# Optimization experiments

Measured on AMD Instinct MI355X. Metric: run time of the kernel, lower is better.

## Reference

```python
import jax, jax.numpy as jnp
import numpy as np

B, H, N, F, P, NODE = 64, 168, 512, 8, 24, 0


def _lstm(x, k, rk, b, return_sequences):
    # x: (B, T, Fin); keras LSTM gate order i, f, g(c), o
    Bx = x.shape[0]
    U = rk.shape[0]
    h0 = jnp.zeros((Bx, U), x.dtype)

    def step(carry, xt):
        h, c = carry
        z = xt @ k + h @ rk + b
        i, f, g, o = jnp.split(z, 4, axis=-1)
        c = jax.nn.sigmoid(f) * c + jax.nn.sigmoid(i) * jnp.tanh(g)
        h = jax.nn.sigmoid(o) * jnp.tanh(c)
        return (h, c), h

    (_, _), hs = jax.lax.scan(step, (h0, h0), jnp.swapaxes(x, 0, 1))
    return jnp.swapaxes(hs, 0, 1) if return_sequences else hs[-1]


def _node_summaries(inputs):
    # inputs: (B, H, N, F). Per-(b,n) temporal stats over H of feature 0.
    x0 = inputs[..., 0]                      # (B, H, N)
    mean_full = x0.mean(axis=1)              # (B, N)
    mean_half = x0[:, H // 2:].mean(axis=1)
    std_full = x0.std(axis=1)                # population std (ddof=0), like tf
    std_half = x0[:, H // 2:].std(axis=1)
    c = x0 - mean_full[:, None, :]
    m2 = (c * c).mean(axis=1)
    m3 = (c ** 3).mean(axis=1)
    m4 = (c ** 4).mean(axis=1)
    skew = jnp.nan_to_num(m3 / m2 ** 1.5)    # scipy.stats.skew (biased)
    kurt = jnp.nan_to_num(m4 / (m2 * m2) - 3.0)  # scipy Fisher kurtosis
    t = jnp.arange(H, dtype=x0.dtype)
    tc = t - t.mean()
    slope = jnp.nan_to_num(jnp.einsum('h,bhn->bn', tc, x0) / (tc * tc).sum())
    return jnp.stack([mean_full, mean_half, std_full, std_half, skew, kurt, slope], axis=2)  # (B, N, 7)


def reference(inputs, adj, w_gcn1, b_gcn1, w_gcn2, b_gcn2, w_conv1, b_conv1,
              w_conv2, b_conv2, k_lstm1, rk_lstm1, b_lstm1, k_lstm2, rk_lstm2,
              b_lstm2, w_out, b_out):
    nf = _node_summaries(inputs)                                   # (B, N, 7)
    # GraphConv: relu(A @ X @ W + b)
    h = jax.nn.relu(jnp.einsum('nm,bmc->bnc', adj, nf @ w_gcn1) + b_gcn1)
    g = jax.nn.relu(jnp.einsum('nm,bmc->bnc', adj, h @ w_gcn2) + b_gcn2)   # (B, N, 16)
    # Conv1D channels_first: channels = N, steps = 16
    dn = ('NCH', 'HIO', 'NCH')
    c1 = jax.lax.conv_general_dilated(g, w_conv1, (1,), 'SAME', dimension_numbers=dn) + b_conv1[None, :, None]  # (B,4,16)
    p = c1.reshape(B, 4, 8, 2).mean(axis=-1)                        # AveragePooling1D(2)  (B,4,8)
    c2 = jax.lax.conv_general_dilated(p, w_conv2, (1,), 'SAME', dimension_numbers=dn) + b_conv2[None, :, None]  # (B,4,8)
    gcn_out = jnp.concatenate([c2.reshape(B, -1), p.reshape(B, -1)], axis=-1)  # skip connection, (B, 64)
    # LSTM stack on the selected node's time series
    seq = inputs[:, :, NODE, :]                                     # (B, H, F)
    l1 = _lstm(seq, k_lstm1, rk_lstm1, b_lstm1, True)
    l2 = _lstm(l1, k_lstm2, rk_lstm2, b_lstm2, False)               # (B, 128)
    out = jnp.concatenate([gcn_out, l2], axis=-1)                   # (B, 192); dropout is identity at inference
    return out @ w_out + b_out                                      # (B, P)


def setup_inputs() -> dict:
    key = jax.random.key(0)
    ks = jax.random.split(key, 16)
    s = 0.05
    return {
        'inputs': jax.random.normal(ks[0], (B, H, N, F), jnp.float32),
        'adj': jax.random.uniform(ks[1], (N, N), jnp.float32) / N,
        'w_gcn1': jax.random.normal(ks[2], (7, 32), jnp.float32) * s,
        'b_gcn1': jnp.zeros((32,), jnp.float32),
        'w_gcn2': jax.random.normal(ks[3], (32, 16), jnp.float32) * s,
        'b_gcn2': jnp.zeros((16,), jnp.float32),
        'w_conv1': jax.random.normal(ks[4], (3, N, 4), jnp.float32) * s,
        'b_conv1': jnp.zeros((4,), jnp.float32),
        'w_conv2': jax.random.normal(ks[5], (3, 4, 4), jnp.float32) * s,
        'b_conv2': jnp.zeros((4,), jnp.float32),
        'k_lstm1': jax.random.normal(ks[6], (F, 512), jnp.float32) * s,
        'rk_lstm1': jax.random.normal(ks[7], (128, 512), jnp.float32) * s,
        'b_lstm1': jnp.zeros((512,), jnp.float32),
        'k_lstm2': jax.random.normal(ks[8], (128, 512), jnp.float32) * s,
        'rk_lstm2': jax.random.normal(ks[9], (128, 512), jnp.float32) * s,
        'b_lstm2': jnp.zeros((512,), jnp.float32),
        'w_out': jax.random.normal(ks[10], (192, P), jnp.float32) * s,
        'b_out': jnp.zeros((P,), jnp.float32),
    }
```

## Files before the change

### kernel.cpp

```cpp
#include <hip/hip_runtime.h>
#include <cstdint>
#include <cstddef>

#define BB 64
#define HH 168
#define NN 512
#define FF 8
#define UL 128
#define GD 512

__device__ __forceinline__ float frcp(float x){ return __builtin_amdgcn_rcpf(x); }
__device__ __forceinline__ void pin4(float4 &v){
  asm volatile("" : "+v"(v.x), "+v"(v.y), "+v"(v.z), "+v"(v.w));
}

__global__ __launch_bounds__(256) void k_sum(const float* __restrict__ in, float* __restrict__ ps){
  int bid = blockIdx.x;
  int b = bid>>2, nh = (bid>>1)&1, hh = bid&1;
  int n = nh*256 + threadIdx.x;
  int h0 = hh*84;
  const float* p = in + ((size_t)(b*HH + h0)*NN + n)*FF;
  float s1=0.f,s2=0.f,s3=0.f,s4=0.f,st=0.f;
  #pragma unroll 4
  for(int h=0;h<84;++h){
    float x = p[(size_t)h*NN*FF];
    float hc = (float)(h+h0) - 83.5f;
    s1 += x;
    float x2 = x*x;
    s2 += x2;
    s3 += x2*x;
    s4 += x2*x2;
    st += hc*x;
  }
  float* o = ps + ((size_t)((b*NN+n)*2 + hh))*8;
  o[0]=s1; o[1]=s2; o[2]=s3; o[3]=s4; o[4]=st;
}

__global__ __launch_bounds__(256) void k_sumc(const float* __restrict__ ps, float* __restrict__ nf){
  int idx = blockIdx.x*256 + threadIdx.x;
  const float* a = ps + (size_t)idx*16;
  const float* c2 = a + 8;
  float s1 = a[0]+c2[0], s2 = a[1]+c2[1], s3 = a[2]+c2[2], s4 = a[3]+c2[3], st = a[4]+c2[4];
  float s1h = c2[0], s2h = c2[1];
  const float iH = 1.0f/168.0f, iHh = 1.0f/84.0f;
  float mean = s1*iH, meanh = s1h*iHh;
  float ex2 = s2*iH, ex3 = s3*iH, ex4 = s4*iH;
  float m2 = ex2 - mean*mean;
  float m3 = ex3 - 3.0f*mean*ex2 + 2.0f*mean*mean*mean;
  float m4 = ex4 - 4.0f*mean*ex3 + 6.0f*mean*mean*ex2 - 3.0f*mean*mean*mean*mean;
  m2 = fmaxf(m2, 0.0f);
  float stdf = sqrtf(m2);
  float m2h = fmaxf(s2h*iHh - meanh*meanh, 0.0f);
  float stdh = sqrtf(m2h);
  float denom = m2*stdf;
  float skew = denom > 0.0f ? m3/denom : 0.0f;
  float kurt = m2 > 0.0f ? (m4/(m2*m2) - 3.0f) : 0.0f;
  float slope = st * (1.0f/395122.0f);
  float* o = nf + (size_t)idx*7;
  o[0]=mean; o[1]=meanh; o[2]=stdf; o[3]=stdh; o[4]=skew; o[5]=kurt; o[6]=slope;
}

__global__ __launch_bounds__(256) void k_gcn1(const float* __restrict__ nf, const float* __restrict__ adj,
        const float* __restrict__ w1, const float* __restrict__ b1, float* __restrict__ h1){
  __shared__ float t_s[NN*32];
  __shared__ float adj_s[128*68];
  int b = blockIdx.x>>2, n0 = (blockIdx.x&3)*128;
  int tid = threadIdx.x;
  {
    int c = tid&31;
    float w1c[7];
    #pragma unroll
    for(int k=0;k<7;++k) w1c[k] = w1[k*32+c];
    for(int idx=tid; idx<NN*32; idx+=256){
      int m = idx>>5;
      const float* nfp = nf + (size_t)(b*NN+m)*7;
      float acc = 0.f;
      #pragma unroll
      for(int k=0;k<7;++k) acc += nfp[k]*w1c[k];
      t_s[idx] = acc;
    }
  }
  int c2 = tid&15, nl = tid>>4;
  float acc[8][2];
  #pragma unroll
  for(int j=0;j<8;++j){acc[j][0]=0.f;acc[j][1]=0.f;}
  for(int mt=0; mt<8; ++mt){
    __syncthreads();
    for(int idx=tid; idx<128*64; idx+=256){
      int r = idx>>6, cc = idx&63;
      adj_s[r*68+cc] = adj[(size_t)(n0+r)*NN + mt*64 + cc];
    }
    __syncthreads();
    for(int mm=0; mm<64; mm+=4){
      float2 tv[4];
      #pragma unroll
      for(int q=0;q<4;++q) tv[q] = *(const float2*)&t_s[(mt*64+mm+q)*32 + 2*c2];
      #pragma unroll
      for(int j=0;j<8;++j){
        float4 a4 = *(const float4*)&adj_s[(nl+16*j)*68 + mm];
        acc[j][0] += a4.x*tv[0].x + a4.y*tv[1].x + a4.z*tv[2].x + a4.w*tv[3].x;
        acc[j][1] += a4.x*tv[0].y + a4.y*tv[1].y + a4.z*tv[2].y + a4.w*tv[3].y;
      }
    }
  }
  float bb0 = b1[2*c2], bb1 = b1[2*c2+1];
  #pragma unroll
  for(int j=0;j<8;++j){
    int n = n0 + nl + 16*j;
    float2 v;
    v.x = fmaxf(acc[j][0]+bb0, 0.0f);
    v.y = fmaxf(acc[j][1]+bb1, 0.0f);
    *(float2*)&h1[(size_t)(b*NN+n)*32 + 2*c2] = v;
  }
}

__global__ __launch_bounds__(256) void k_gcn2(const float* __restrict__ h1, const float* __restrict__ adj,
        const float* __restrict__ w2, const float* __restrict__ b2, float* __restrict__ g){
  __shared__ float t_s[NN*16];
  __shared__ float adj_s[128*68];
  int b = blockIdx.x>>2, n0 = (blockIdx.x&3)*128;
  int tid = threadIdx.x;
  {
    int jh = tid&7;
    float w2c0[32], w2c1[32];
    #pragma unroll
    for(int c=0;c<32;++c){ w2c0[c] = w2[c*16+2*jh]; w2c1[c] = w2[c*16+2*jh+1]; }
    for(int idx=tid; idx<NN*8; idx+=256){
      int m = idx>>3;
      const float4* hp = (const float4*)(h1 + (size_t)(b*NN+m)*32);
      float a0=0.f, a1=0.f;
      #pragma unroll
      for(int q=0;q<8;++q){
        float4 hv = hp[q];
        a0 += hv.x*w2c0[4*q] + hv.y*w2c0[4*q+1] + hv.z*w2c0[4*q+2] + hv.w*w2c0[4*q+3];
        a1 += hv.x*w2c1[4*q] + hv.y*w2c1[4*q+1] + hv.z*w2c1[4*q+2] + hv.w*w2c1[4*q+3];
      }
      t_s[m*16+2*jh] = a0;
      t_s[m*16+2*jh+1] = a1;
    }
  }
  int j = tid&15, nl = tid>>4;
  float acc[8];
  #pragma unroll
  for(int q=0;q<8;++q) acc[q]=0.f;
  for(int mt=0; mt<8; ++mt){
    __syncthreads();
    for(int idx=tid; idx<128*64; idx+=256){
      int r = idx>>6, cc = idx&63;
      adj_s[r*68+cc] = adj[(size_t)(n0+r)*NN + mt*64 + cc];
    }
    __syncthreads();
    for(int mm=0; mm<64; mm+=4){
      float tv[4];
      #pragma unroll
      for(int q=0;q<4;++q) tv[q] = t_s[(mt*64+mm+q)*16 + j];
      #pragma unroll
      for(int q=0;q<8;++q){
        float4 a4 = *(const float4*)&adj_s[(nl+16*q)*68 + mm];
        acc[q] += a4.x*tv[0] + a4.y*tv[1] + a4.z*tv[2] + a4.w*tv[3];
      }
    }
  }
  float bbj = b2[j];
  #pragma unroll
  for(int q=0;q<8;++q){
    int n = n0 + nl + 16*q;
    g[(size_t)(b*NN+n)*16 + j] = fmaxf(acc[q]+bbj, 0.0f);
  }
}

__global__ __launch_bounds__(256) void k_conv(const float* __restrict__ g, const float* __restrict__ wc1,
        const float* __restrict__ bc1, const float* __restrict__ wc2, const float* __restrict__ bc2,
        float* __restrict__ feat){
  __shared__ float g_s[NN*16];
  __shared__ float w1_s[3*NN*4];
  __shared__ float c1p[4][4][16];
  __shared__ float c1_s[4][16];
  __shared__ float p_s[4][8];
  int b = blockIdx.x, tid = threadIdx.x;
  for(int idx=tid; idx<NN*16; idx+=256) g_s[idx] = g[(size_t)b*NN*16 + idx];
  for(int idx=tid; idx<3*NN*4; idx+=256) w1_s[idx] = wc1[idx];
  __syncthreads();
  {
    int q = tid>>6, p = tid&63, o = p>>4, x = p&15;
    int c0 = q*128;
    float acc = 0.f;
    #pragma unroll
    for(int k=0;k<3;++k){
      int xx = x + k - 1;
      if(xx>=0 && xx<16){
        #pragma unroll 4
        for(int c=c0;c<c0+128;++c) acc += g_s[c*16+xx]*w1_s[(k*NN+c)*4+o];
      }
    }
    c1p[q][o][x] = acc;
  }
  __syncthreads();
  if(tid<64){
    int o = tid>>4, x = tid&15;
    c1_s[o][x] = c1p[0][o][x]+c1p[1][o][x]+c1p[2][o][x]+c1p[3][o][x] + bc1[o];
  }
  __syncthreads();
  if(tid<32){
    int oo = tid>>3, xp = tid&7;
    float pv = 0.5f*(c1_s[oo][2*xp]+c1_s[oo][2*xp+1]);
    p_s[oo][xp] = pv;
    feat[b*192 + 32 + oo*8 + xp] = pv;
  }
  __syncthreads();
  if(tid<32){
    int oo = tid>>3, x2 = tid&7;
    float a2 = bc2[oo];
    #pragma unroll
    for(int k=0;k<3;++k){
      int xx = x2 + k - 1;
      if(xx>=0 && xx<8){
        #pragma unroll
        for(int c=0;c<4;++c) a2 += p_s[c][xx]*wc2[(k*4+c)*4+oo];
      }
    }
    feat[b*192 + oo*8 + x2] = a2;
  }
}

__global__ __launch_bounds__(256) void k_xk1(const float* __restrict__ in, const float* __restrict__ k1,
        const float* __restrict__ b1, float* __restrict__ zin){
  __shared__ float x_s[21*FF];
  int b = blockIdx.x>>3, t0 = (blockIdx.x&7)*21;
  int tid = threadIdx.x;
  for(int idx=tid; idx<21*FF; idx+=256)
    x_s[idx] = in[(size_t)(b*HH + t0 + (idx>>3))*NN*FF + (idx&7)];
  __syncthreads();
  float acc0[21], acc1[21];
  #pragma unroll
  for(int q=0;q<21;++q){acc0[q]=0.f;acc1[q]=0.f;}
  #pragma unroll
  for(int j=0;j<FF;++j){
    float kv0 = k1[j*GD + tid];
    float kv1 = k1[j*GD + tid + 256];
    #pragma unroll
    for(int q=0;q<21;++q){
      float xv = x_s[q*FF + j];
      acc0[q] += xv*kv0;
      acc1[q] += xv*kv1;
    }
  }
  float bb0 = b1[tid], bb1 = b1[tid+256];
  #pragma unroll
  for(int q=0;q<21;++q){
    zin[((size_t)b*HH + t0 + q)*GD + tid]       = acc0[q] + bb0;
    zin[((size_t)b*HH + t0 + q)*GD + tid + 256] = acc1[q] + bb1;
  }
}

__global__ __launch_bounds__(256) void k_zin2(const float* __restrict__ l1, const float* __restrict__ k2,
        const float* __restrict__ b2, float* __restrict__ zin){
  __shared__ float l_s[21*UL];
  int b = blockIdx.x>>3, t0 = (blockIdx.x&7)*21;
  int tid = threadIdx.x;
  for(int idx=tid; idx<21*UL; idx+=256)
    l_s[idx] = l1[((size_t)b*HH + t0 + (idx>>7))*UL + (idx&127)];
  __syncthreads();
  float acc0[21], acc1[21];
  #pragma unroll
  for(int q=0;q<21;++q){acc0[q]=0.f;acc1[q]=0.f;}
  for(int j=0;j<UL;j+=4){
    float kv00=k2[j*GD+tid],     kv01=k2[(j+1)*GD+tid],     kv02=k2[(j+2)*GD+tid],     kv03=k2[(j+3)*GD+tid];
    float kv10=k2[j*GD+tid+256], kv11=k2[(j+1)*GD+tid+256], kv12=k2[(j+2)*GD+tid+256], kv13=k2[(j+3)*GD+tid+256];
    #pragma unroll
    for(int q=0;q<21;++q){
      float4 lv = *(const float4*)&l_s[q*UL + j];
      acc0[q] += lv.x*kv00 + lv.y*kv01 + lv.z*kv02 + lv.w*kv03;
      acc1[q] += lv.x*kv10 + lv.y*kv11 + lv.z*kv12 + lv.w*kv13;
    }
  }
  float bb0 = b2[tid], bb1 = b2[tid+256];
  #pragma unroll
  for(int q=0;q<21;++q){
    zin[((size_t)b*HH + t0 + q)*GD + tid]       = acc0[q] + bb0;
    zin[((size_t)b*HH + t0 + q)*GD + tid + 256] = acc1[q] + bb1;
  }
}

__global__ __launch_bounds__(1024,4) __attribute__((amdgpu_waves_per_eu(4,4)))
void k_rec(const float* __restrict__ zin, const float* __restrict__ rk,
           float* __restrict__ oseq, float* __restrict__ olast, int writeSeq){
  __shared__ float hbuf[2][8*20];
  int b = blockIdx.x, tid = threadIdx.x;
  int w = tid>>6, l = tid&63;
  int gate = l>>4;
  int ks = l&7;
  int b3 = (l>>3)&1;
  int cbase = gate*128 + w*8 + b3*4;
  int col = cbase + (l&3);
  int u = w*8 + b3*4 + (l&3);
  bool q0 = (l&1)!=0, q1 = (l&2)!=0;
  bool wr = (gate==0) && ((l&4)==0);

  float4 w4[16];
  #pragma unroll
  for(int k=0;k<16;++k)
    w4[k] = *(const float4*)(rk + (size_t)(ks*16+k)*GD + cbase);
  #pragma unroll
  for(int k=0;k<16;++k) pin4(w4[k]);

  bool isg = (gate==2);
  float Ac = isg?1.f:0.f, Bc = isg?-2.f:1.f, Sc = isg?2.f:-1.f;

  if(tid<UL) hbuf[0][(tid>>4)*20 + (tid&15)] = 0.0f;
  float c = 0.0f;
  float zc = zin[(size_t)b*HH*GD + col];
  __syncthreads();

  int cur = 0;
  #pragma unroll 1
  for(int t=0;t<HH;++t){
    float nz = 0.f;
    if(t+1<HH) nz = zin[((size_t)b*HH + t+1)*GD + col];
    const float4* hq = (const float4*)&hbuf[cur][ks*20];
    float p0=0.f,p1=0.f,p2=0.f,p3=0.f;
    #pragma unroll
    for(int j=0;j<4;++j){
      float4 hv = hq[j];
      p0 += hv.x*w4[4*j].x + hv.y*w4[4*j+1].x + hv.z*w4[4*j+2].x + hv.w*w4[4*j+3].x;
      p1 += hv.x*w4[4*j].y + hv.y*w4[4*j+1].y + hv.z*w4[4*j+2].y + hv.w*w4[4*j+3].y;
      p2 += hv.x*w4[4*j].z + hv.y*w4[4*j+1].z + hv.z*w4[4*j+2].z + hv.w*w4[4*j+3].z;
      p3 += hv.x*w4[4*j].w + hv.y*w4[4*j+1].w + hv.z*w4[4*j+2].w + hv.w*w4[4*j+3].w;
    }
    p0 += __shfl_xor(p0,4); p1 += __shfl_xor(p1,4);
    p2 += __shfl_xor(p2,4); p3 += __shfl_xor(p3,4);
    float send0 = q0 ? p0 : p1;
    float send1 = q0 ? p2 : p3;
    float r0 = __shfl_xor(send0, 1);
    float r1 = __shfl_xor(send1, 1);
    float s0 = (q0 ? p1 : p0) + r0;
    float s1v = (q0 ? p3 : p2) + r1;
    float send2 = q1 ? s0 : s1v;
    float r2 = __shfl_xor(send2, 2);
    float z = zc + (q1 ? s1v : s0) + r2;
    float act = Ac + Bc*frcp(1.0f + __expf(Sc*z));
    float r16 = __shfl_xor(act, 16);
    float r32 = __shfl_xor(act, 32);
    float r48 = __shfl_xor(r16, 32);
    float ia = gate==0?act : gate==1?r16 : gate==2?r32 : r48;
    float fa = gate==0?r16 : gate==1?act : gate==2?r48 : r32;
    float ga = gate==0?r32 : gate==1?r48 : gate==2?act : r16;
    float oa = gate==0?r48 : gate==1?r32 : gate==2?r16 : act;
    c = fa*c + ia*ga;
    float th = 1.0f - 2.0f*frcp(1.0f + __expf(2.0f*c));
    float hn = oa*th;
    if(wr){
      hbuf[cur^1][(u>>4)*20 + (u&15)] = hn;
      if(writeSeq) oseq[((size_t)b*HH + t)*UL + u] = hn;
      else if(t==HH-1) olast[b*192 + 64 + u] = hn;
    }
    __syncthreads();
    cur ^= 1;
    zc = nz;
  }
}

__global__ __launch_bounds__(256) void k_out(const float* __restrict__ feat, const float* __restrict__ wo,
        const float* __restrict__ bo, float* __restrict__ out){
  int idx = blockIdx.x*256 + threadIdx.x;
  if(idx >= BB*24) return;
  int b = idx/24, p = idx - b*24;
  float a0 = bo[p], a1 = 0.f, a2 = 0.f, a3 = 0.f;
  const float* f = feat + b*192;
  for(int k=0;k<192;k+=4){
    a0 += f[k]*wo[k*24+p];
    a1 += f[k+1]*wo[(k+1)*24+p];
    a2 += f[k+2]*wo[(k+2)*24+p];
    a3 += f[k+3]*wo[(k+3)*24+p];
  }
  out[idx] = (a0+a1)+(a2+a3);
}

extern "C" void kernel_launch(void* const* d_in, const int* in_sizes, int n_in,
                              void* d_out, int out_size, void* d_ws, size_t ws_size,
                              hipStream_t stream){
  const float* inp = (const float*)d_in[0];
  const float* adj = (const float*)d_in[1];
  const float* w1  = (const float*)d_in[2];
  const float* b1  = (const float*)d_in[3];
  const float* w2  = (const float*)d_in[4];
  const float* b2  = (const float*)d_in[5];
  const float* wc1 = (const float*)d_in[6];
  const float* bc1 = (const float*)d_in[7];
  const float* wc2 = (const float*)d_in[8];
  const float* bc2 = (const float*)d_in[9];
  const float* k1  = (const float*)d_in[10];
  const float* rk1 = (const float*)d_in[11];
  const float* bl1 = (const float*)d_in[12];
  const float* k2  = (const float*)d_in[13];
  const float* rk2 = (const float*)d_in[14];
  const float* bl2 = (const float*)d_in[15];
  const float* wo  = (const float*)d_in[16];
  const float* bo  = (const float*)d_in[17];
  float* out = (float*)d_out;
  float* ws = (float*)d_ws;

  float* ps   = ws;
  float* nf   = ps + 524288;
  float* h1   = nf + 229376;
  float* g    = h1 + 1048576;
  float* feat = g  + 524288;
  float* l1   = feat + 12288;
  float* zin  = l1 + 1376256;

  k_sum  <<<dim3(256), dim3(256), 0, stream>>>(inp, ps);
  k_sumc <<<dim3(128), dim3(256), 0, stream>>>(ps, nf);
  k_gcn1 <<<dim3(256), dim3(256), 0, stream>>>(nf, adj, w1, b1, h1);
  k_gcn2 <<<dim3(256), dim3(256), 0, stream>>>(h1, adj, w2, b2, g);
  k_conv <<<dim3(64),  dim3(256), 0, stream>>>(g, wc1, bc1, wc2, bc2, feat);
  k_xk1  <<<dim3(512), dim3(256), 0, stream>>>(inp, k1, bl1, zin);
  k_rec  <<<dim3(64),  dim3(1024),0, stream>>>(zin, rk1, l1, feat, 1);
  k_zin2 <<<dim3(512), dim3(256), 0, stream>>>(l1, k2, bl2, zin);
  k_rec  <<<dim3(64),  dim3(1024),0, stream>>>(zin, rk2, l1, feat, 0);
  k_out  <<<dim3(6),   dim3(256), 0, stream>>>(feat, wo, bo, out);
}
```

Baseline: 500.3 us.

## Halve LSTM recurrence block size and exchange gate activations through LDS

```diff
diff --git a/kernel.cpp b/kernel.cpp
--- a/kernel.cpp
+++ b/kernel.cpp
@@ -282,53 +282,48 @@
   }
 }
 
-__global__ __launch_bounds__(1024,4) __attribute__((amdgpu_waves_per_eu(4,4)))
+__global__ __launch_bounds__(512) __attribute__((amdgpu_waves_per_eu(2,2)))
 void k_rec(const float* __restrict__ zin, const float* __restrict__ rk,
            float* __restrict__ oseq, float* __restrict__ olast, int writeSeq){
-  __shared__ float hbuf[2][8*20];
+  __shared__ float hbuf[2][4*36];
+  __shared__ float a_s[UL*4];
   int b = blockIdx.x, tid = threadIdx.x;
-  int w = tid>>6, l = tid&63;
-  int gate = l>>4;
-  int ks = l&7;
-  int b3 = (l>>3)&1;
-  int cbase = gate*128 + w*8 + b3*4;
-  int col = cbase + (l&3);
-  int u = w*8 + b3*4 + (l&3);
-  bool q0 = (l&1)!=0, q1 = (l&2)!=0;
-  bool wr = (gate==0) && ((l&4)==0);
-
-  float4 w4[16];
-  #pragma unroll
-  for(int k=0;k<16;++k)
-    w4[k] = *(const float4*)(rk + (size_t)(ks*16+k)*GD + cbase);
-  #pragma unroll
-  for(int k=0;k<16;++k) pin4(w4[k]);
-
+  int q = tid&3, grp = tid>>2;
+  int gate = tid>>7;
+  int u = tid&127;
+  bool q0 = (tid&1)!=0, q1 = (tid&2)!=0;
+
+  float4 w4[32];
+  {
+    const float4* rkp = (const float4*)rk;
+    #pragma unroll
+    for(int k=0;k<32;++k) w4[k] = rkp[(size_t)(q*32+k)*(GD/4) + grp];
+    #pragma unroll
+    for(int k=0;k<32;++k) pin4(w4[k]);
+  }
   bool isg = (gate==2);
   float Ac = isg?1.f:0.f, Bc = isg?-2.f:1.f, Sc = isg?2.f:-1.f;
 
-  if(tid<UL) hbuf[0][(tid>>4)*20 + (tid&15)] = 0.0f;
+  if(tid<UL) hbuf[0][(tid>>5)*36 + (tid&31)] = 0.0f;
   float c = 0.0f;
-  float zc = zin[(size_t)b*HH*GD + col];
+  float zc = zin[(size_t)b*HH*GD + tid];
   __syncthreads();
 
   int cur = 0;
   #pragma unroll 1
   for(int t=0;t<HH;++t){
     float nz = 0.f;
-    if(t+1<HH) nz = zin[((size_t)b*HH + t+1)*GD + col];
-    const float4* hq = (const float4*)&hbuf[cur][ks*20];
+    if(t+1<HH) nz = zin[((size_t)b*HH + t+1)*GD + tid];
+    const float4* hq = (const float4*)&hbuf[cur][q*36];
     float p0=0.f,p1=0.f,p2=0.f,p3=0.f;
     #pragma unroll
-    for(int j=0;j<4;++j){
+    for(int j=0;j<8;++j){
       float4 hv = hq[j];
       p0 += hv.x*w4[4*j].x + hv.y*w4[4*j+1].x + hv.z*w4[4*j+2].x + hv.w*w4[4*j+3].x;
       p1 += hv.x*w4[4*j].y + hv.y*w4[4*j+1].y + hv.z*w4[4*j+2].y + hv.w*w4[4*j+3].y;
       p2 += hv.x*w4[4*j].z + hv.y*w4[4*j+1].z + hv.z*w4[4*j+2].z + hv.w*w4[4*j+3].z;
       p3 += hv.x*w4[4*j].w + hv.y*w4[4*j+1].w + hv.z*w4[4*j+2].w + hv.w*w4[4*j+3].w;
     }
-    p0 += __shfl_xor(p0,4); p1 += __shfl_xor(p1,4);
-    p2 += __shfl_xor(p2,4); p3 += __shfl_xor(p3,4);
     float send0 = q0 ? p0 : p1;
     float send1 = q0 ? p2 : p3;
     float r0 = __shfl_xor(send0, 1);
@@ -339,18 +334,14 @@
     float r2 = __shfl_xor(send2, 2);
     float z = zc + (q1 ? s1v : s0) + r2;
     float act = Ac + Bc*frcp(1.0f + __expf(Sc*z));
-    float r16 = __shfl_xor(act, 16);
-    float r32 = __shfl_xor(act, 32);
-    float r48 = __shfl_xor(r16, 32);
-    float ia = gate==0?act : gate==1?r16 : gate==2?r32 : r48;
-    float fa = gate==0?r16 : gate==1?act : gate==2?r48 : r32;
-    float ga = gate==0?r32 : gate==1?r48 : gate==2?act : r16;
-    float oa = gate==0?r48 : gate==1?r32 : gate==2?r16 : act;
-    c = fa*c + ia*ga;
+    a_s[u*4 + gate] = act;
+    __syncthreads();
+    float4 a4 = *(const float4*)&a_s[u*4];
+    c = a4.y*c + a4.x*a4.z;
     float th = 1.0f - 2.0f*frcp(1.0f + __expf(2.0f*c));
-    float hn = oa*th;
-    if(wr){
-      hbuf[cur^1][(u>>4)*20 + (u&15)] = hn;
+    float hn = a4.w*th;
+    if(tid<UL){
+      hbuf[cur^1][(u>>5)*36 + (u&31)] = hn;
       if(writeSeq) oseq[((size_t)b*HH + t)*UL + u] = hn;
       else if(t==HH-1) olast[b*192 + 64 + u] = hn;
     }
@@ -414,8 +405,8 @@
   k_gcn2 <<<dim3(256), dim3(256), 0, stream>>>(h1, adj, w2, b2, g);
   k_conv <<<dim3(64),  dim3(256), 0, stream>>>(g, wc1, bc1, wc2, bc2, feat);
   k_xk1  <<<dim3(512), dim3(256), 0, stream>>>(inp, k1, bl1, zin);
-  k_rec  <<<dim3(64),  dim3(1024),0, stream>>>(zin, rk1, l1, feat, 1);
+  k_rec  <<<dim3(64),  dim3(512), 0, stream>>>(zin, rk1, l1, feat, 1);
   k_zin2 <<<dim3(512), dim3(256), 0, stream>>>(l1, k2, bl2, zin);
-  k_rec  <<<dim3(64),  dim3(1024),0, stream>>>(zin, rk2, l1, feat, 0);
+  k_rec  <<<dim3(64),  dim3(512), 0, stream>>>(zin, rk2, l1, feat, 0);
   k_out  <<<dim3(6),   dim3(256), 0, stream>>>(feat, wo, bo, out);
 }
```

Result: faster. 443.7 us (-11.3%).
